# Performance work log

Measured on AMD Instinct MI355X. Metric: run time of the kernel, lower is better.

## Reference

```python
import jax, jax.numpy as jnp
import numpy as np

EMBED_DIM = 512
NUM_HEADS = 8
HEAD_DIM = EMBED_DIM // NUM_HEADS
SCALING = HEAD_DIM ** (-0.5)
LAMBDA = 1.0
T = 128
B = 8


def setup_inputs() -> dict:
    key = jax.random.key(0)
    ks = jax.random.split(key, 8)
    d = EMBED_DIM
    # xavier-uniform-ish scale for weights
    w_lim = float(np.sqrt(6.0 / (3 * d + d)))
    o_lim = float(np.sqrt(6.0 / (d + d)))
    return {
        "query": jax.random.normal(ks[0], (T, B, d), jnp.float32),
        "key": jax.random.normal(ks[1], (T, B, d), jnp.float32),
        "value": jax.random.normal(ks[2], (T, B, d), jnp.float32),
        "correlation_bias": jax.random.normal(ks[3], (B, T, T, T), jnp.float32) * 0.1,
        "in_proj_weight": jax.random.uniform(ks[4], (3 * d, d), jnp.float32, -w_lim, w_lim),
        "in_proj_bias": jnp.zeros((3 * d,), jnp.float32),
        "out_w": jax.random.uniform(ks[5], (d, d), jnp.float32, -o_lim, o_lim),
        "out_b": jnp.zeros((d,), jnp.float32),
    }


def reference(query, key, value, correlation_bias, in_proj_weight, in_proj_bias, out_w, out_b):
    tgt_len, bsz, d = query.shape
    h, hd = NUM_HEADS, HEAD_DIM
    # split packed in-projection
    q = query @ in_proj_weight[:d].T + in_proj_bias[:d]
    k = key @ in_proj_weight[d:2 * d].T + in_proj_bias[d:2 * d]
    v = value @ in_proj_weight[2 * d:].T + in_proj_bias[2 * d:]
    q = q * SCALING
    # [T, B, D] -> [B*H, T, hd]
    q = q.reshape(tgt_len, bsz * h, hd).transpose(1, 0, 2)
    k = k.reshape(tgt_len, bsz * h, hd).transpose(1, 0, 2)
    v = v.reshape(tgt_len, bsz * h, hd).transpose(1, 0, 2)
    # trilinear score cube: [B*H, Tq, Tk, Tv]
    scores = jnp.einsum('iat,ibt,ict->iabc', q, k, v)
    # expand correlation bias over heads: [B,Tq,Tk,Tv] -> [B*H,Tq,Tk,Tv]
    bias = jnp.broadcast_to(
        correlation_bias[:, None], (bsz, h, tgt_len, tgt_len, tgt_len)
    ).reshape(bsz * h, tgt_len, tgt_len, tgt_len)
    scores = scores + LAMBDA * bias
    # mean/max fusion over Tv, softmax over Tk
    fused = jnp.mean(scores, axis=-1) + jnp.max(scores, axis=-1)
    w = jax.nn.softmax(fused.astype(jnp.float32), axis=-1).astype(fused.dtype)
    # bmm with q (note: attends over q itself, Tk == Tq required)
    attn = jnp.einsum('iab,ibd->iad', w, q)
    attn = attn.transpose(1, 0, 2).reshape(tgt_len, bsz, d)
    return attn @ out_w.T + out_b
```

## Files before the change

### kernel.cpp

```cpp
#include <hip/hip_runtime.h>
#include <math.h>

#define SCALING 0.125f

typedef __attribute__((ext_vector_type(8))) short short8;
typedef __attribute__((ext_vector_type(4))) float f32x4;

static __device__ __forceinline__ unsigned short bf16r(float x) {
  unsigned int u = __float_as_uint(x);
  u += 0x7fffu + ((u >> 16) & 1u);
  return (unsigned short)(u >> 16);
}
static __device__ __forceinline__ float bf16f(unsigned short h) {
  return __uint_as_float(((unsigned int)h) << 16);
}
static __device__ __forceinline__ unsigned int pk_bf16(float lo, float hi) {
  unsigned int ua = __float_as_uint(lo);
  unsigned int ub = __float_as_uint(hi);
  ua += 0x7fffu + ((ua >> 16) & 1u);
  ub += 0x7fffu + ((ub >> 16) & 1u);
  return __builtin_amdgcn_perm(ub, ua, 0x07060302u);
}
static __device__ __forceinline__ void split4(float4 x, ushort4& h, ushort4& l) {
  h.x = bf16r(x.x); l.x = bf16r(x.x - bf16f(h.x));
  h.y = bf16r(x.y); l.y = bf16r(x.y - bf16f(h.y));
  h.z = bf16r(x.z); l.z = bf16r(x.z - bf16f(h.z));
  h.w = bf16r(x.w); l.w = bf16r(x.w - bf16f(h.w));
}
union U4S8 { uint4 u; short8 s; };

__global__ __launch_bounds__(256)
void projmm_kernel(const float* __restrict__ query,
                   const float* __restrict__ key,
                   const float* __restrict__ value,
                   const float* __restrict__ W,
                   const float* __restrict__ bias,
                   float* __restrict__ qh, float* __restrict__ kh,
                   unsigned short* __restrict__ vh) {
  __shared__ __align__(16) unsigned short Ah[64 * 72];
  __shared__ __align__(16) unsigned short Al[64 * 72];
  __shared__ __align__(16) unsigned short Bh[64 * 72];
  __shared__ __align__(16) unsigned short Bl[64 * 72];
  const int n0 = blockIdx.x * 64;
  const int g = n0 >> 9;
  const float* __restrict__ X = (g == 0) ? query : (g == 1) ? key : value;
  const int m0 = blockIdx.y * 64;
  const int tid = threadIdx.x;
  const int w = tid >> 6, lane = tid & 63;
  const int quad = lane >> 4, n15 = lane & 15;
  const int srow = tid >> 2;
  const int scol = (tid & 3) * 16;

  f32x4 acc[4];
#pragma unroll
  for (int nt = 0; nt < 4; ++nt) acc[nt] = (f32x4){0.f, 0.f, 0.f, 0.f};

  float4 av[4], bv[4];
#pragma unroll
  for (int jj = 0; jj < 4; ++jj) {
    av[jj] = *(const float4*)&X[(m0 + srow) * 512 + scol + 4 * jj];
    bv[jj] = *(const float4*)&W[(n0 + srow) * 512 + scol + 4 * jj];
  }

  for (int k0 = 0; k0 < 512; k0 += 64) {
    __syncthreads();
#pragma unroll
    for (int jj = 0; jj < 4; ++jj) {
      ushort4 hh, ll;
      split4(av[jj], hh, ll);
      *(ushort4*)&Ah[srow * 72 + scol + 4 * jj] = hh;
      *(ushort4*)&Al[srow * 72 + scol + 4 * jj] = ll;
      split4(bv[jj], hh, ll);
      *(ushort4*)&Bh[srow * 72 + scol + 4 * jj] = hh;
      *(ushort4*)&Bl[srow * 72 + scol + 4 * jj] = ll;
    }
    __syncthreads();
    if (k0 + 64 < 512) {
#pragma unroll
      for (int jj = 0; jj < 4; ++jj) {
        av[jj] = *(const float4*)&X[(m0 + srow) * 512 + k0 + 64 + scol + 4 * jj];
        bv[jj] = *(const float4*)&W[(n0 + srow) * 512 + k0 + 64 + scol + 4 * jj];
      }
    }
#pragma unroll
    for (int kk = 0; kk < 2; ++kk) {
      short8 ah = *(const short8*)&Ah[(w * 16 + n15) * 72 + kk * 32 + quad * 8];
      short8 al = *(const short8*)&Al[(w * 16 + n15) * 72 + kk * 32 + quad * 8];
#pragma unroll
      for (int nt = 0; nt < 4; ++nt) {
        short8 bh = *(const short8*)&Bh[(nt * 16 + n15) * 72 + kk * 32 + quad * 8];
        short8 bl = *(const short8*)&Bl[(nt * 16 + n15) * 72 + kk * 32 + quad * 8];
        acc[nt] = __builtin_amdgcn_mfma_f32_16x16x32_bf16(ah, bh, acc[nt], 0, 0, 0);
        acc[nt] = __builtin_amdgcn_mfma_f32_16x16x32_bf16(ah, bl, acc[nt], 0, 0, 0);
        acc[nt] = __builtin_amdgcn_mfma_f32_16x16x32_bf16(al, bh, acc[nt], 0, 0, 0);
      }
    }
  }

#pragma unroll
  for (int nt = 0; nt < 4; ++nt) {
    const int j = n0 + nt * 16 + n15;
    const int jj = j & 511;
    const int head = jj >> 6;
    const int hd = jj & 63;
    const float bj = bias[j];
#pragma unroll
    for (int r = 0; r < 4; ++r) {
      const int row = m0 + w * 16 + quad * 4 + r;
      const int t = row >> 3;
      const int batch = row & 7;
      const int i = batch * 8 + head;
      const int idx = ((i << 7) + t) * 64 + hd;
      const float val = acc[nt][r] + bj;
      if (g == 0)      qh[idx] = val * SCALING;
      else if (g == 1) kh[idx] = val;
      else             vh[idx] = bf16r(val);
    }
  }
}

__global__ __launch_bounds__(256, 2)
void score_kernel(const float* __restrict__ qh,
                  const float* __restrict__ kh,
                  const unsigned short* __restrict__ vh,
                  const float* __restrict__ cbias,
                  float* __restrict__ fused) {
  __shared__ __align__(16) unsigned short Ks[2][128 * 72];
  __shared__ __align__(16) unsigned short Vs[2][128 * 72];

  const int ab = blockIdx.x;
  const int batch = ab >> 7;
  const int a = ab & 127;
  const int tid = threadIdx.x;
  const int w = tid >> 6;
  const int lane = tid & 63;
  const int quad = lane >> 4;
  const int n15 = lane & 15;
  const int col8 = (tid & 7) * 8;

  const float* __restrict__ bp = cbias + (size_t)ab * 16384;
  f32x4 biasReg[8][2];
#pragma unroll
  for (int ic = 0; ic < 8; ++ic)
#pragma unroll
    for (int jb = 0; jb < 2; ++jb) {
      const int b = w * 32 + jb * 16 + n15;
      biasReg[ic][jb] = *(const f32x4*)&bp[b * 128 + ic * 16 + quad * 4];
    }

  {
    const int i = batch * 8;
    const float* __restrict__ kb = kh + (size_t)i * 8192;
    const uint4* __restrict__ vb4 = (const uint4*)(vh + (size_t)i * 8192);
    const float* __restrict__ qa = qh + ((size_t)i * 128 + a) * 64;
    f32x4 q0 = *(const f32x4*)&qa[col8];
    f32x4 q1 = *(const f32x4*)&qa[col8 + 4];
#pragma unroll
    for (int j = 0; j < 4; ++j) {
      const int gg = j * 256 + tid;
      const int row = gg >> 3;
      *(uint4*)&Vs[0][row * 72 + col8] = vb4[gg];
      f32x4 k0 = *(const f32x4*)&kb[8 * gg];
      f32x4 k1 = *(const f32x4*)&kb[8 * gg + 4];
      k0 *= q0;
      k1 *= q1;
      uint4 pk;
      pk.x = pk_bf16(k0[0], k0[1]); pk.y = pk_bf16(k0[2], k0[3]);
      pk.z = pk_bf16(k1[0], k1[1]); pk.w = pk_bf16(k1[2], k1[3]);
      *(uint4*)&Ks[0][row * 72 + col8] = pk;
    }
  }
  __syncthreads();

  for (int h = 0; h < 8; ++h) {
    const int buf = h & 1;
    const int i = batch * 8 + h;

    uint4 vreg[4];
    f32x4 kreg[4][2];
    f32x4 qn0, qn1;
    if (h < 7) {
      const int in = i + 1;
      const float* __restrict__ kb = kh + (size_t)in * 8192;
      const uint4* __restrict__ vb4 = (const uint4*)(vh + (size_t)in * 8192);
      const float* __restrict__ qa = qh + ((size_t)in * 128 + a) * 64;
      qn0 = *(const f32x4*)&qa[col8];
      qn1 = *(const f32x4*)&qa[col8 + 4];
#pragma unroll
      for (int j = 0; j < 4; ++j) {
        const int gg = j * 256 + tid;
        vreg[j] = vb4[gg];
        kreg[j][0] = *(const f32x4*)&kb[8 * gg];
        kreg[j][1] = *(const f32x4*)&kb[8 * gg + 4];
      }
    }

    short8 bf[2][2];
#pragma unroll
    for (int jb = 0; jb < 2; ++jb)
#pragma unroll
      for (int kk = 0; kk < 2; ++kk)
        bf[jb][kk] = *(const short8*)&Ks[buf][(w * 32 + jb * 16 + n15) * 72 +
                                             kk * 32 + quad * 8];

    f32x4 acc[8][2];
#pragma unroll
    for (int ic = 0; ic < 8; ++ic)
#pragma unroll
      for (int jb = 0; jb < 2; ++jb) acc[ic][jb] = (f32x4){0.f, 0.f, 0.f, 0.f};
#pragma unroll
    for (int ic = 0; ic < 8; ++ic) {
      short8 a0 = *(const short8*)&Vs[buf][(ic * 16 + n15) * 72 + quad * 8];
      short8 a1 = *(const short8*)&Vs[buf][(ic * 16 + n15) * 72 + 32 + quad * 8];
      acc[ic][0] = __builtin_amdgcn_mfma_f32_16x16x32_bf16(a0, bf[0][0], acc[ic][0], 0, 0, 0);
      acc[ic][0] = __builtin_amdgcn_mfma_f32_16x16x32_bf16(a1, bf[0][1], acc[ic][0], 0, 0, 0);
      acc[ic][1] = __builtin_amdgcn_mfma_f32_16x16x32_bf16(a0, bf[1][0], acc[ic][1], 0, 0, 0);
      acc[ic][1] = __builtin_amdgcn_mfma_f32_16x16x32_bf16(a1, bf[1][1], acc[ic][1], 0, 0, 0);
    }

    if (h < 7) {
      const int nb = buf ^ 1;
#pragma unroll
      for (int j = 0; j < 4; ++j) {
        const int gg = j * 256 + tid;
        const int row = gg >> 3;
        *(uint4*)&Vs[nb][row * 72 + col8] = vreg[j];
        kreg[j][0] *= qn0;
        kreg[j][1] *= qn1;
        uint4 pk;
        pk.x = pk_bf16(kreg[j][0][0], kreg[j][0][1]);
        pk.y = pk_bf16(kreg[j][0][2], kreg[j][0][3]);
        pk.z = pk_bf16(kreg[j][1][0], kreg[j][1][1]);
        pk.w = pk_bf16(kreg[j][1][2], kreg[j][1][3]);
        *(uint4*)&Ks[nb][row * 72 + col8] = pk;
      }
    }

    float fsum[2] = {0.f, 0.f};
    float fmx[2] = {-INFINITY, -INFINITY};
#pragma unroll
    for (int ic = 0; ic < 8; ++ic)
#pragma unroll
      for (int jb = 0; jb < 2; ++jb) {
        const float v0 = acc[ic][jb][0] + biasReg[ic][jb][0];
        const float v1 = acc[ic][jb][1] + biasReg[ic][jb][1];
        const float v2 = acc[ic][jb][2] + biasReg[ic][jb][2];
        const float v3 = acc[ic][jb][3] + biasReg[ic][jb][3];
        fsum[jb] += (v0 + v1) + (v2 + v3);
        fmx[jb] = fmaxf(fmx[jb], fmaxf(fmaxf(v0, v1), fmaxf(v2, v3)));
      }
#pragma unroll
    for (int off = 16; off <= 32; off <<= 1) {
#pragma unroll
      for (int jb = 0; jb < 2; ++jb) {
        fsum[jb] += __shfl_xor(fsum[jb], off, 64);
        fmx[jb] = fmaxf(fmx[jb], __shfl_xor(fmx[jb], off, 64));
      }
    }
    if (quad == 0) {
      float* fo = fused + ((size_t)i * 128 + a) * 128 + w * 32;
      fo[n15] = fsum[0] * (1.0f / 128.0f) + fmx[0];
      fo[16 + n15] = fsum[1] * (1.0f / 128.0f) + fmx[1];
    }

    __syncthreads();
  }
}

__global__ __launch_bounds__(64)
void softmax_attn_kernel(const float* __restrict__ fused,
                         const float* __restrict__ qh,
                         float* __restrict__ attn) {
  const int bid = blockIdx.x;
  const int i = bid >> 7;
  const int a = bid & 127;
  const int lane = threadIdx.x;
  const float* __restrict__ fr = fused + (size_t)bid * 128;
  float f0 = fr[lane], f1 = fr[lane + 64];
  float m = fmaxf(f0, f1);
#pragma unroll
  for (int off = 32; off >= 1; off >>= 1) m = fmaxf(m, __shfl_xor(m, off, 64));
  const float e0 = expf(f0 - m), e1 = expf(f1 - m);
  float s = e0 + e1;
#pragma unroll
  for (int off = 32; off >= 1; off >>= 1) s += __shfl_xor(s, off, 64);
  const float inv = 1.0f / s;
  __shared__ float w[128];
  w[lane] = e0 * inv;
  w[lane + 64] = e1 * inv;
  __syncthreads();
  const float* __restrict__ qp = qh + (size_t)i * 128 * 64 + lane;
  float acc = 0.0f;
#pragma unroll 4
  for (int b = 0; b < 128; b++) acc = fmaf(w[b], qp[b * 64], acc);
  const int batch = i >> 3, head = i & 7;
  attn[((size_t)a * 8 + batch) * 512 + head * 64 + lane] = acc;
}

__global__ __launch_bounds__(256)
void outmm_kernel(const float* __restrict__ Xa,
                  const float* __restrict__ W,
                  const float* __restrict__ bias,
                  float* __restrict__ out) {
  __shared__ __align__(16) unsigned short Ah[64 * 72];
  __shared__ __align__(16) unsigned short Al[64 * 72];
  __shared__ __align__(16) unsigned short Bh[64 * 72];
  __shared__ __align__(16) unsigned short Bl[64 * 72];
  const int n0 = blockIdx.x * 64;
  const int m0 = blockIdx.y * 64;
  const int tid = threadIdx.x;
  const int w = tid >> 6, lane = tid & 63;
  const int quad = lane >> 4, n15 = lane & 15;
  const int srow = tid >> 2;
  const int scol = (tid & 3) * 16;

  f32x4 acc[4];
#pragma unroll
  for (int nt = 0; nt < 4; ++nt) acc[nt] = (f32x4){0.f, 0.f, 0.f, 0.f};

  float4 av[4], bv[4];
#pragma unroll
  for (int jj = 0; jj < 4; ++jj) {
    av[jj] = *(const float4*)&Xa[(m0 + srow) * 512 + scol + 4 * jj];
    bv[jj] = *(const float4*)&W[(n0 + srow) * 512 + scol + 4 * jj];
  }

  for (int k0 = 0; k0 < 512; k0 += 64) {
    __syncthreads();
#pragma unroll
    for (int jj = 0; jj < 4; ++jj) {
      ushort4 hh, ll;
      split4(av[jj], hh, ll);
      *(ushort4*)&Ah[srow * 72 + scol + 4 * jj] = hh;
      *(ushort4*)&Al[srow * 72 + scol + 4 * jj] = ll;
      split4(bv[jj], hh, ll);
      *(ushort4*)&Bh[srow * 72 + scol + 4 * jj] = hh;
      *(ushort4*)&Bl[srow * 72 + scol + 4 * jj] = ll;
    }
    __syncthreads();
    if (k0 + 64 < 512) {
#pragma unroll
      for (int jj = 0; jj < 4; ++jj) {
        av[jj] = *(const float4*)&Xa[(m0 + srow) * 512 + k0 + 64 + scol + 4 * jj];
        bv[jj] = *(const float4*)&W[(n0 + srow) * 512 + k0 + 64 + scol + 4 * jj];
      }
    }
#pragma unroll
    for (int kk = 0; kk < 2; ++kk) {
      short8 ah = *(const short8*)&Ah[(w * 16 + n15) * 72 + kk * 32 + quad * 8];
      short8 al = *(const short8*)&Al[(w * 16 + n15) * 72 + kk * 32 + quad * 8];
#pragma unroll
      for (int nt = 0; nt < 4; ++nt) {
        short8 bh = *(const short8*)&Bh[(nt * 16 + n15) * 72 + kk * 32 + quad * 8];
        short8 bl = *(const short8*)&Bl[(nt * 16 + n15) * 72 + kk * 32 + quad * 8];
        acc[nt] = __builtin_amdgcn_mfma_f32_16x16x32_bf16(ah, bh, acc[nt], 0, 0, 0);
        acc[nt] = __builtin_amdgcn_mfma_f32_16x16x32_bf16(ah, bl, acc[nt], 0, 0, 0);
        acc[nt] = __builtin_amdgcn_mfma_f32_16x16x32_bf16(al, bh, acc[nt], 0, 0, 0);
      }
    }
  }

#pragma unroll
  for (int nt = 0; nt < 4; ++nt) {
    const int j = n0 + nt * 16 + n15;
    const float bj = bias[j];
#pragma unroll
    for (int r = 0; r < 4; ++r) {
      const int row = m0 + w * 16 + quad * 4 + r;
      out[(size_t)row * 512 + j] = acc[nt][r] + bj;
    }
  }
}

extern "C" void kernel_launch(void* const* d_in, const int* in_sizes, int n_in,
                              void* d_out, int out_size, void* d_ws,
                              size_t ws_size, hipStream_t stream) {
  const float* query = (const float*)d_in[0];
  const float* key   = (const float*)d_in[1];
  const float* value = (const float*)d_in[2];
  const float* cbias = (const float*)d_in[3];
  const float* W     = (const float*)d_in[4];
  const float* pb    = (const float*)d_in[5];
  const float* out_w = (const float*)d_in[6];
  const float* out_b = (const float*)d_in[7];
  float* out = (float*)d_out;

  float* ws = (float*)d_ws;
  float* qh = ws;
  float* kh = ws + 524288;
  unsigned short* vh = (unsigned short*)(ws + 1048576);
  float* fusedb = ws + 1048576 + 262144;
  float* attn = fusedb + 1048576;

  projmm_kernel<<<dim3(24, 16), 256, 0, stream>>>(query, key, value, W, pb,
                                                  qh, kh, vh);
  score_kernel<<<1024, 256, 0, stream>>>(qh, kh, vh, cbias, fusedb);
  softmax_attn_kernel<<<8192, 64, 0, stream>>>(fusedb, qh, attn);
  outmm_kernel<<<dim3(8, 16), 256, 0, stream>>>(attn, out_w, out_b, out);
}
```

Before: 185.6 us.

## Fuse softmax and attention bmm into score kernel; halve outmm N tile

The separate softmax_attn kernel is folded into the tail of score_kernel. Each block keeps its fused mean+max rows for all heads in shared memory, then every wave runs softmax and the weighted sum over q for two heads. This drops the fused-score round trip through global memory and one kernel launch, at the cost of extra serial work and 4KB more shared memory per score block. The output projection also moves to 32-column tiles, doubling the grid, with only half the threads loading W.

Result: no change. 185.3 us (-0.2%).

```diff
diff --git a/kernel.cpp b/kernel.cpp
--- a/kernel.cpp
+++ b/kernel.cpp
@@ -124,9 +124,10 @@
                   const float* __restrict__ kh,
                   const unsigned short* __restrict__ vh,
                   const float* __restrict__ cbias,
-                  float* __restrict__ fused) {
+                  float* __restrict__ attn) {
   __shared__ __align__(16) unsigned short Ks[2][128 * 72];
   __shared__ __align__(16) unsigned short Vs[2][128 * 72];
+  __shared__ float rowS[8 * 128];
 
   const int ab = blockIdx.x;
   const int batch = ab >> 7;
@@ -258,43 +259,35 @@
       }
     }
     if (quad == 0) {
-      float* fo = fused + ((size_t)i * 128 + a) * 128 + w * 32;
-      fo[n15] = fsum[0] * (1.0f / 128.0f) + fmx[0];
-      fo[16 + n15] = fsum[1] * (1.0f / 128.0f) + fmx[1];
+      rowS[h * 128 + w * 32 + n15] = fsum[0] * (1.0f / 128.0f) + fmx[0];
+      rowS[h * 128 + w * 32 + 16 + n15] = fsum[1] * (1.0f / 128.0f) + fmx[1];
     }
 
     __syncthreads();
   }
-}
-
-__global__ __launch_bounds__(64)
-void softmax_attn_kernel(const float* __restrict__ fused,
-                         const float* __restrict__ qh,
-                         float* __restrict__ attn) {
-  const int bid = blockIdx.x;
-  const int i = bid >> 7;
-  const int a = bid & 127;
-  const int lane = threadIdx.x;
-  const float* __restrict__ fr = fused + (size_t)bid * 128;
-  float f0 = fr[lane], f1 = fr[lane + 64];
-  float m = fmaxf(f0, f1);
-#pragma unroll
-  for (int off = 32; off >= 1; off >>= 1) m = fmaxf(m, __shfl_xor(m, off, 64));
-  const float e0 = expf(f0 - m), e1 = expf(f1 - m);
-  float s = e0 + e1;
-#pragma unroll
-  for (int off = 32; off >= 1; off >>= 1) s += __shfl_xor(s, off, 64);
-  const float inv = 1.0f / s;
-  __shared__ float w[128];
-  w[lane] = e0 * inv;
-  w[lane + 64] = e1 * inv;
-  __syncthreads();
-  const float* __restrict__ qp = qh + (size_t)i * 128 * 64 + lane;
-  float acc = 0.0f;
-#pragma unroll 4
-  for (int b = 0; b < 128; b++) acc = fmaf(w[b], qp[b * 64], acc);
-  const int batch = i >> 3, head = i & 7;
-  attn[((size_t)a * 8 + batch) * 512 + head * 64 + lane] = acc;
+
+#pragma unroll
+  for (int hh = 0; hh < 2; ++hh) {
+    const int h = w * 2 + hh;
+    const int i = batch * 8 + h;
+    float f0 = rowS[h * 128 + lane], f1 = rowS[h * 128 + 64 + lane];
+    float m = fmaxf(f0, f1);
+#pragma unroll
+    for (int off = 32; off >= 1; off >>= 1) m = fmaxf(m, __shfl_xor(m, off, 64));
+    const float e0 = expf(f0 - m), e1 = expf(f1 - m);
+    float s = e0 + e1;
+#pragma unroll
+    for (int off = 32; off >= 1; off >>= 1) s += __shfl_xor(s, off, 64);
+    const float inv = 1.0f / s;
+    rowS[h * 128 + lane] = e0 * inv;
+    rowS[h * 128 + 64 + lane] = e1 * inv;
+    const float* __restrict__ qp = qh + (size_t)i * 8192 + lane;
+    float acc2 = 0.0f;
+#pragma unroll 8
+    for (int b = 0; b < 128; ++b)
+      acc2 = fmaf(rowS[h * 128 + b], qp[b * 64], acc2);
+    attn[((size_t)a * 8 + batch) * 512 + h * 64 + lane] = acc2;
+  }
 }
 
 __global__ __launch_bounds__(256)
@@ -304,25 +297,31 @@
                   float* __restrict__ out) {
   __shared__ __align__(16) unsigned short Ah[64 * 72];
   __shared__ __align__(16) unsigned short Al[64 * 72];
-  __shared__ __align__(16) unsigned short Bh[64 * 72];
-  __shared__ __align__(16) unsigned short Bl[64 * 72];
-  const int n0 = blockIdx.x * 64;
+  __shared__ __align__(16) unsigned short Bh[32 * 72];
+  __shared__ __align__(16) unsigned short Bl[32 * 72];
+  const int n0 = blockIdx.x * 32;
   const int m0 = blockIdx.y * 64;
   const int tid = threadIdx.x;
   const int w = tid >> 6, lane = tid & 63;
   const int quad = lane >> 4, n15 = lane & 15;
   const int srow = tid >> 2;
   const int scol = (tid & 3) * 16;
-
-  f32x4 acc[4];
-#pragma unroll
-  for (int nt = 0; nt < 4; ++nt) acc[nt] = (f32x4){0.f, 0.f, 0.f, 0.f};
+  const bool doB = tid >= 128;
+  const int brow = (tid & 127) >> 2;
+  const int bcol = (tid & 3) * 16;
+
+  f32x4 acc[2];
+#pragma unroll
+  for (int nt = 0; nt < 2; ++nt) acc[nt] = (f32x4){0.f, 0.f, 0.f, 0.f};
 
   float4 av[4], bv[4];
 #pragma unroll
-  for (int jj = 0; jj < 4; ++jj) {
+  for (int jj = 0; jj < 4; ++jj)
     av[jj] = *(const float4*)&Xa[(m0 + srow) * 512 + scol + 4 * jj];
-    bv[jj] = *(const float4*)&W[(n0 + srow) * 512 + scol + 4 * jj];
+  if (doB) {
+#pragma unroll
+    for (int jj = 0; jj < 4; ++jj)
+      bv[jj] = *(const float4*)&W[(n0 + brow) * 512 + bcol + 4 * jj];
   }
 
   for (int k0 = 0; k0 < 512; k0 += 64) {
@@ -333,16 +332,25 @@
       split4(av[jj], hh, ll);
       *(ushort4*)&Ah[srow * 72 + scol + 4 * jj] = hh;
       *(ushort4*)&Al[srow * 72 + scol + 4 * jj] = ll;
-      split4(bv[jj], hh, ll);
-      *(ushort4*)&Bh[srow * 72 + scol + 4 * jj] = hh;
-      *(ushort4*)&Bl[srow * 72 + scol + 4 * jj] = ll;
+    }
+    if (doB) {
+#pragma unroll
+      for (int jj = 0; jj < 4; ++jj) {
+        ushort4 hh, ll;
+        split4(bv[jj], hh, ll);
+        *(ushort4*)&Bh[brow * 72 + bcol + 4 * jj] = hh;
+        *(ushort4*)&Bl[brow * 72 + bcol + 4 * jj] = ll;
+      }
     }
     __syncthreads();
     if (k0 + 64 < 512) {
 #pragma unroll
-      for (int jj = 0; jj < 4; ++jj) {
+      for (int jj = 0; jj < 4; ++jj)
         av[jj] = *(const float4*)&Xa[(m0 + srow) * 512 + k0 + 64 + scol + 4 * jj];
-        bv[jj] = *(const float4*)&W[(n0 + srow) * 512 + k0 + 64 + scol + 4 * jj];
+      if (doB) {
+#pragma unroll
+        for (int jj = 0; jj < 4; ++jj)
+          bv[jj] = *(const float4*)&W[(n0 + brow) * 512 + k0 + 64 + bcol + 4 * jj];
       }
     }
 #pragma unroll
@@ -350,7 +358,7 @@
       short8 ah = *(const short8*)&Ah[(w * 16 + n15) * 72 + kk * 32 + quad * 8];
       short8 al = *(const short8*)&Al[(w * 16 + n15) * 72 + kk * 32 + quad * 8];
 #pragma unroll
-      for (int nt = 0; nt < 4; ++nt) {
+      for (int nt = 0; nt < 2; ++nt) {
         short8 bh = *(const short8*)&Bh[(nt * 16 + n15) * 72 + kk * 32 + quad * 8];
         short8 bl = *(const short8*)&Bl[(nt * 16 + n15) * 72 + kk * 32 + quad * 8];
         acc[nt] = __builtin_amdgcn_mfma_f32_16x16x32_bf16(ah, bh, acc[nt], 0, 0, 0);
@@ -361,7 +369,7 @@
   }
 
 #pragma unroll
-  for (int nt = 0; nt < 4; ++nt) {
+  for (int nt = 0; nt < 2; ++nt) {
     const int j = n0 + nt * 16 + n15;
     const float bj = bias[j];
 #pragma unroll
@@ -389,12 +397,10 @@
   float* qh = ws;
   float* kh = ws + 524288;
   unsigned short* vh = (unsigned short*)(ws + 1048576);
-  float* fusedb = ws + 1048576 + 262144;
-  float* attn = fusedb + 1048576;
+  float* attn = ws + 1048576 + 262144;
 
   projmm_kernel<<<dim3(24, 16), 256, 0, stream>>>(query, key, value, W, pb,
                                                   qh, kh, vh);
-  score_kernel<<<1024, 256, 0, stream>>>(qh, kh, vh, cbias, fusedb);
-  softmax_attn_kernel<<<8192, 64, 0, stream>>>(fusedb, qh, attn);
-  outmm_kernel<<<dim3(8, 16), 256, 0, stream>>>(attn, out_w, out_b, out);
-}
+  score_kernel<<<1024, 256, 0, stream>>>(qh, kh, vh, cbias, attn);
+  outmm_kernel<<<dim3(16, 16), 256, 0, stream>>>(attn, out_w, out_b, out);
+}
```
